# Kernel optimization log

Measured on AMD Instinct MI355X. Metric: run time of the kernel, lower is better.

Reference implementation:

```python
import math
import jax, jax.numpy as jnp
import numpy as np

IN_CH = 64
NUM_ANCHOR = 4
MAP_H, MAP_W = 96, 96
BATCH = 8
BN_EPS = 1e-5


def _conv2d(x, w, b, padding, dilation):
    # x: [B,C,H,W], w: [O,I,kh,kw] (OIHW)
    y = jax.lax.conv_general_dilated(
        x, w, window_strides=(1, 1),
        padding=((padding, padding), (padding, padding)),
        rhs_dilation=(dilation, dilation),
        dimension_numbers=('NCHW', 'OIHW', 'NCHW'))
    return y + b[None, :, None, None]


def _bn(x, gamma, beta, mean, var):
    scale = gamma / jnp.sqrt(var + BN_EPS)
    return x * scale[None, :, None, None] + (beta - mean * scale)[None, :, None, None]


def setup_inputs() -> dict:
    key = jax.random.key(0)
    ks = jax.random.split(key, 12)
    # cyclic channel-shift permutation matrices, one per anchor pass
    eye = np.eye(IN_CH, dtype=np.float32)
    shift = IN_CH // (2 * NUM_ANCHOR)
    perms = np.stack([eye[np.roll(np.arange(IN_CH), i * shift)] for i in range(2 * NUM_ANCHOR)])
    w_std = 1.0 / math.sqrt(IN_CH * 9)
    return {
        'x': jax.random.normal(ks[0], (BATCH, IN_CH, MAP_H, MAP_W), dtype=jnp.float32),
        'perms': jnp.asarray(perms),
        'dcn_w': jax.random.normal(ks[1], (IN_CH, IN_CH, 3, 3), dtype=jnp.float32) * w_std,
        'dcn_b': jax.random.normal(ks[2], (IN_CH,), dtype=jnp.float32) * 0.01,
        'conv2_w': jax.random.normal(ks[3], (IN_CH, IN_CH, 3, 3), dtype=jnp.float32) * w_std,
        'conv2_b': jax.random.normal(ks[4], (IN_CH,), dtype=jnp.float32) * 0.01,
        'conv3_w': jax.random.normal(ks[5], (IN_CH, IN_CH, 3, 3), dtype=jnp.float32) * w_std,
        'conv3_b': jax.random.normal(ks[6], (IN_CH,), dtype=jnp.float32) * 0.01,
        'bn_gamma': jax.random.uniform(ks[7], (3, IN_CH), dtype=jnp.float32, minval=0.5, maxval=1.5),
        'bn_beta': jax.random.normal(ks[8], (3, IN_CH), dtype=jnp.float32) * 0.1,
        'bn_mean': jax.random.normal(ks[9], (3, IN_CH), dtype=jnp.float32) * 0.1,
        'bn_var': jax.random.uniform(ks[10], (3, IN_CH), dtype=jnp.float32, minval=0.5, maxval=1.5),
    }


def reference(x, perms, dcn_w, dcn_b, conv2_w, conv2_b, conv3_w, conv3_b,
              bn_gamma, bn_beta, bn_mean, bn_var):
    h = x.shape[2]
    pad = math.ceil(h / (2 ** 1.5 + 2))  # 20 for h=96

    def conv_stack(o):
        # DCN at init (zero offsets) == plain 3x3 conv, pad=1
        o = jax.nn.relu(_bn(_conv2d(o, dcn_w, dcn_b, 1, 1), bn_gamma[0], bn_beta[0], bn_mean[0], bn_var[0]))
        o = jax.nn.relu(_bn(_conv2d(o, conv2_w, conv2_b, 2, 2), bn_gamma[1], bn_beta[1], bn_mean[1], bn_var[1]))
        o = jax.nn.relu(_bn(_conv2d(o, conv3_w, conv3_b, 2, 2), bn_gamma[2], bn_beta[2], bn_mean[2], bn_var[2]))
        return o

    outs = []
    for i in range(2 * NUM_ANCHOR):  # fixed small structural loop
        o = jnp.einsum('mn,bnhw->bmhw', perms[i], x)  # channel permutation
        if i % 2 != 0:
            o = jnp.pad(o, ((0, 0), (0, 0), (pad, pad), (pad, pad)))
        o = jnp.rot90(o, k=i % 4, axes=(-2, -1))   # ccw rotate
        o = conv_stack(o)
        o = jnp.rot90(o, k=(-i) % 4, axes=(-2, -1))  # cw rotate back
        if i % 2 != 0:
            H, W = o.shape[-2], o.shape[-1]
            sh, sw = (H - MAP_H) // 2, (W - MAP_W) // 2
            o = o[..., sh:sh + MAP_H, sw:sw + MAP_W]  # center crop
        outs.append(o)
    out_tensor = jnp.concatenate(outs, axis=1)  # [B, 8*C, H, W]
    out = jnp.max(out_tensor, axis=1, keepdims=True)
    # branch_name == 'midpoint', orientational_anchor=False -> clamped sigmoid
    return jnp.clip(jax.nn.sigmoid(out), 1e-4, 1.0 - 1e-4)
```

## Files before the change

kernel.cpp:

```cpp
#include <hip/hip_runtime.h>
#include <math.h>

#define B 8
#define C 64
#define HW 96
#define NWV 36864

typedef __attribute__((ext_vector_type(8)))  short short8;
typedef __attribute__((ext_vector_type(16))) float floatx16;

__device__ __forceinline__ unsigned short f2bf(float f) {
    unsigned int u = __float_as_uint(f);
    unsigned int r = (u + 0x7fffu + ((u >> 16) & 1u)) >> 16;
    return (unsigned short)r;
}

__device__ __forceinline__ void rotmap(int k, int ta, int tb, int& sa, int& sb) {
    switch (k) {
        case 0: sa = ta;     sb = tb;     break;
        case 1: sa = 2 - tb; sb = ta;     break;
        case 2: sa = 2 - ta; sb = 2 - tb; break;
        default: sa = tb;    sb = 2 - ta; break;
    }
}

__global__ void prep_w(const float* __restrict__ dcn_w, const float* __restrict__ c2w,
                       const float* __restrict__ c3w,
                       const float* __restrict__ gamma, const float* __restrict__ var_,
                       unsigned short* __restrict__ Wall) {
    int idx = blockIdx.x * 256 + threadIdx.x;
    if (idx >= 16 * NWV) return;
    int v = idx / NWV, rem = idx % NWV;
    int tap  = rem >> 12;
    int w12  = rem & 4095;
    int ks   = w12 >> 10;
    int cf   = (w12 >> 9) & 1;
    int lane = (w12 >> 3) & 63;
    int j    = w12 & 7;
    int co = cf * 32 + (lane & 31);
    int ci = ks * 16 + (lane >> 5) * 8 + j;
    int ta = tap / 3, tb = tap % 3;
    const float* src; int k, srcci, l;
    if (v < 8)       { k = v & 3;  srcci = (ci + 8 * v) & 63; src = dcn_w; l = 0; }
    else if (v < 12) { k = v - 8;  srcci = ci; src = c2w; l = 1; }
    else             { k = v - 12; srcci = ci; src = c3w; l = 2; }
    int sa, sb; rotmap(k, ta, tb, sa, sb);
    float s = gamma[l * 64 + co] * rsqrtf(var_[l * 64 + co] + 1e-5f);
    Wall[idx] = f2bf(src[((co * 64 + srcci) * 3 + sa) * 3 + sb] * s);
}

__global__ void prep_bias(const float* __restrict__ dcn_b, const float* __restrict__ c2b,
                          const float* __restrict__ c3b,
                          const float* __restrict__ gamma, const float* __restrict__ beta,
                          const float* __restrict__ mean, const float* __restrict__ var_,
                          float* __restrict__ biasg) {
    int t = threadIdx.x;
    if (t < 192) {
        int l = t >> 6, c = t & 63;
        const float* cb = (l == 0) ? dcn_b : ((l == 1) ? c2b : c3b);
        float s = gamma[l * 64 + c] * rsqrtf(var_[l * 64 + c] + 1e-5f);
        biasg[t] = cb[c] * s + beta[l * 64 + c] - mean[l * 64 + c] * s;
    }
}

__global__ __launch_bounds__(256) void prep_x(const float* __restrict__ in,
                                              unsigned short* __restrict__ out) {
    __shared__ float row[64 * 97];
    int by = blockIdx.x;
    int b = by / 96, y = by % 96;
    int t = threadIdx.x;
    for (int e = t; e < 6144; e += 256) {
        int c = e / 96, x = e - c * 96;
        row[c * 97 + x] = in[(((size_t)(b * 64 + c) * 96 + y) * 96) + x];
    }
    __syncthreads();
    for (int e = t; e < 6144; e += 256) {
        int x = e >> 6, c = e & 63;
        out[(((size_t)(b * 96 + y) * 96 + x) << 6) + c] = f2bf(row[c * 97 + x]);
    }
}

__global__ __launch_bounds__(256) void border_clear(unsigned short* __restrict__ buf1) {
    int idx = blockIdx.y;
    int br = (idx >> 3) * 2, b = idx & 7;
    int z = br * 8 + b;
    int i = blockIdx.x * 32 + (threadIdx.x >> 3);
    int g = threadIdx.x & 7;
    int r, c;
    if (i < 416)      { r = i / 104;              c = i % 104; }
    else if (i < 832) { int j = i - 416; r = 100 + j / 104; c = j % 104; }
    else              { int j = i - 832; r = 4 + (j >> 3); int c8 = j & 7;
                        c = (c8 < 4) ? c8 : 92 + c8; }
    uint4 zero = make_uint4(0u, 0u, 0u, 0u);
    *(uint4*)(buf1 + (size_t)z * (104 * 104 * 64) + ((size_t)(r * 104 + c) << 6) + (g << 3)) = zero;
}

__global__ __launch_bounds__(256, 2) void conv1_k(
    const unsigned short* __restrict__ xhwc, unsigned short* __restrict__ buf1,
    const unsigned short* __restrict__ Wall, const float* __restrict__ biasg) {

    __shared__ __align__(16) unsigned short xt[10 * 34 * 64];

    int z = blockIdx.z, br = z >> 3, b = z & 7, odd = br & 1;
    int fy0 = blockIdx.y * 8, fx0 = blockIdx.x * 32;
    int t = threadIdx.x, lane = t & 63, wv = t >> 6;
    int n = lane & 31, kq = lane >> 5;

    const unsigned short* xb = xhwc + ((size_t)b * 96 * 96 << 6);
    const short8* Ag = (const short8*)(Wall + (size_t)br * NWV);

    for (int e = t; e < 2720; e += 256) {
        int p = e >> 3, g = e & 7;
        int yy = p / 34, xx = p - yy * 34;
        int gy = fy0 - 5 + yy, gx = fx0 - 5 + xx;
        uint4 v = make_uint4(0u, 0u, 0u, 0u);
        if ((unsigned)gy < 96u && (unsigned)gx < 96u)
            v = *(const uint4*)(xb + ((size_t)(gy * 96 + gx) << 6) + (g << 3));
        *(uint4*)(xt + (p << 6) + ((g ^ (xx & 7)) << 3)) = v;
    }
    __syncthreads();

    floatx16 acc[2][2];
#pragma unroll
    for (int cf = 0; cf < 2; cf++)
#pragma unroll
        for (int pf = 0; pf < 2; pf++)
#pragma unroll
            for (int i = 0; i < 16; i++) acc[cf][pf][i] = 0.f;

#pragma unroll
    for (int ks = 0; ks < 4; ks++) {
#pragma unroll
        for (int tb = 0; tb < 3; tb++) {
            short8 a[3][2];
#pragma unroll
            for (int ta = 0; ta < 3; ta++)
#pragma unroll
                for (int cf = 0; cf < 2; cf++)
                    a[ta][cf] = Ag[(((ta * 3 + tb) * 4 + ks) * 2 + cf) * 64 + lane];
            int xx = n + tb;
            int g = ((ks * 2 + kq) ^ (xx & 7)) << 3;
            short8 bf[4];
#pragma unroll
            for (int rr = 0; rr < 4; rr++) {
                int p = (2 * wv + rr) * 34 + xx;
                bf[rr] = *(const short8*)(xt + (p << 6) + g);
            }
#pragma unroll
            for (int ta = 0; ta < 3; ta++)
#pragma unroll
                for (int pf = 0; pf < 2; pf++) {
                    int rr = pf + ta;
                    acc[0][pf] = __builtin_amdgcn_mfma_f32_32x32x16_bf16(a[ta][0], bf[rr], acc[0][pf], 0, 0, 0);
                    acc[1][pf] = __builtin_amdgcn_mfma_f32_32x32x16_bf16(a[ta][1], bf[rr], acc[1][pf], 0, 0, 0);
                }
        }
    }

    float4 bv[2][4];
#pragma unroll
    for (int cf = 0; cf < 2; cf++)
#pragma unroll
        for (int rb = 0; rb < 4; rb++)
            bv[cf][rb] = *(const float4*)(biasg + 32 * cf + 8 * rb + 4 * kq);

    __syncthreads();
#pragma unroll
    for (int pf = 0; pf < 2; pf++) {
        int pq = (2 * wv + pf) * 32 + n;
        int key = (pq & 7) << 1;
#pragma unroll
        for (int cf = 0; cf < 2; cf++)
#pragma unroll
            for (int rb = 0; rb < 4; rb++) {
                int u = kq + 2 * rb + 8 * cf;
                float v0 = fmaxf(acc[cf][pf][rb * 4 + 0] + bv[cf][rb].x, 0.f);
                float v1 = fmaxf(acc[cf][pf][rb * 4 + 1] + bv[cf][rb].y, 0.f);
                float v2 = fmaxf(acc[cf][pf][rb * 4 + 2] + bv[cf][rb].z, 0.f);
                float v3 = fmaxf(acc[cf][pf][rb * 4 + 3] + bv[cf][rb].w, 0.f);
                uint2 pk = make_uint2((unsigned)f2bf(v0) | ((unsigned)f2bf(v1) << 16),
                                      (unsigned)f2bf(v2) | ((unsigned)f2bf(v3) << 16));
                *(uint2*)((char*)xt + pq * 128 + ((u ^ key) << 3)) = pk;
            }
    }
    __syncthreads();

    unsigned short* fb = buf1 + (size_t)z * (104 * 104 * 64);
    int lo = odd ? 0 : 4, hi = odd ? 104 : 100;
    for (int e = t; e < 2048; e += 256) {
        int px = e >> 3, g = e & 7;
        int key = (px & 7) << 1;
        uint4 v = *(const uint4*)((const char*)xt + px * 128 + (((2 * g) ^ key) << 3));
        int lr = px >> 5, nn = px & 31;
        int f = fy0 + lr, fc = fx0 + nn;
        if (f >= lo && f < hi && fc >= lo && fc < hi)
            *(uint4*)(fb + ((size_t)(f * 104 + fc) << 6) + (g << 3)) = v;
    }
}

__global__ __launch_bounds__(512, 2) void conv23_k(
    const unsigned short* __restrict__ buf1, float* __restrict__ maxb,
    const unsigned short* __restrict__ Wall, const float* __restrict__ biasg) {

    __shared__ __align__(16) unsigned short c2out[768 * 64];
    __shared__ __align__(16) unsigned short xs[960 * 32];

    int z = blockIdx.z, br = z >> 3, odd = br & 1;
    int oy0 = blockIdx.y * 16, ox0 = blockIdx.x * 32;
    int t = threadIdx.x, lane = t & 63, wv = t >> 6;
    int n = lane & 31, kq = lane >> 5;

    const unsigned short* fb = buf1 + (size_t)z * (104 * 104 * 64);
    const short8* A2 = (const short8*)(Wall + (size_t)(8  + (br & 3)) * NWV);
    const short8* A3 = (const short8*)(Wall + (size_t)(12 + (br & 3)) * NWV);

    for (int e = t; e < 3840; e += 512) {
        int p = e >> 2, g = e & 3;
        int yy = p / 40, xx = p - yy * 40;
        uint4 v = *(const uint4*)(fb + ((size_t)((oy0 + yy) * 104 + ox0 + xx) << 6) + (g << 3));
        *(uint4*)(xs + (p << 5) + ((g ^ (xx & 3)) << 3)) = v;
    }
    __syncthreads();

    uint4 pfv[8];
#pragma unroll
    for (int k = 0; k < 8; k++) {
        int e = t + k * 512;
        if (e < 3840) {
            int p = e >> 2, g = e & 3;
            int yy = p / 40, xx = p - yy * 40;
            pfv[k] = *(const uint4*)(fb + ((size_t)((oy0 + yy) * 104 + ox0 + xx) << 6) + 32 + (g << 3));
        }
    }

    int q_[3], row2_[3], col2_[3];
#pragma unroll
    for (int jj = 0; jj < 3; jj++) {
        int q = 96 * wv + 32 * jj + n;
        q_[jj] = q;
        int qc = (q < 720) ? q : 719;
        int r2 = qc / 36;
        row2_[jj] = r2;
        col2_[jj] = qc - 36 * r2;
    }

    floatx16 acc2[3][2];
#pragma unroll
    for (int jj = 0; jj < 3; jj++)
#pragma unroll
        for (int cf = 0; cf < 2; cf++)
#pragma unroll
            for (int i = 0; i < 16; i++) acc2[jj][cf][i] = 0.f;

#pragma unroll
    for (int s = 0; s < 2; s++) {
        if (s == 1) {
            __syncthreads();
#pragma unroll
            for (int k = 0; k < 8; k++) {
                int e = t + k * 512;
                if (e < 3840) {
                    int p = e >> 2, g = e & 3;
                    int xx2 = p - (p / 40) * 40;
                    *(uint4*)(xs + (p << 5) + ((g ^ (xx2 & 3)) << 3)) = pfv[k];
                }
            }
            __syncthreads();
        }
#pragma unroll
        for (int kl = 0; kl < 2; kl++) {
            int ks = s * 2 + kl;
#pragma unroll
            for (int tb = 0; tb < 3; tb++) {
                short8 a[3][2];
#pragma unroll
                for (int ta = 0; ta < 3; ta++)
#pragma unroll
                    for (int cf = 0; cf < 2; cf++)
                        a[ta][cf] = A2[(((ta * 3 + tb) * 4 + ks) * 2 + cf) * 64 + lane];
#pragma unroll
                for (int jj = 0; jj < 3; jj++) {
                    int colx = col2_[jj] + 2 * tb;
                    int gsw = ((kl * 2 + kq) ^ (colx & 3)) << 3;
#pragma unroll
                    for (int ta = 0; ta < 3; ta++) {
                        int p = (row2_[jj] + 2 * ta) * 40 + colx;
                        short8 bfr = *(const short8*)(xs + (p << 5) + gsw);
                        acc2[jj][0] = __builtin_amdgcn_mfma_f32_32x32x16_bf16(a[ta][0], bfr, acc2[jj][0], 0, 0, 0);
                        acc2[jj][1] = __builtin_amdgcn_mfma_f32_32x32x16_bf16(a[ta][1], bfr, acc2[jj][1], 0, 0, 0);
                    }
                }
            }
        }
    }

    int rlo2 = (!odd && oy0 == 0)  ? 2  : 0;
    int rhi2 = (!odd && oy0 == 80) ? 18 : 20;
    int clo2 = (!odd && ox0 == 0)  ? 2  : 0;
    int chi2 = (!odd && ox0 == 64) ? 34 : 36;
    float4 bv2[2][4];
#pragma unroll
    for (int cf = 0; cf < 2; cf++)
#pragma unroll
        for (int rb = 0; rb < 4; rb++)
            bv2[cf][rb] = *(const float4*)(biasg + 64 + 32 * cf + 8 * rb + 4 * kq);

#pragma unroll
    for (int jj = 0; jj < 3; jj++) {
        if (q_[jj] < 720) {
            bool valid = (row2_[jj] >= rlo2) && (row2_[jj] < rhi2) &&
                         (col2_[jj] >= clo2) && (col2_[jj] < chi2);
            int key = col2_[jj] & 14;
#pragma unroll
            for (int cf = 0; cf < 2; cf++)
#pragma unroll
                for (int rb = 0; rb < 4; rb++) {
                    int u = kq + 2 * rb + 8 * cf;
                    float v0 = 0.f, v1 = 0.f, v2 = 0.f, v3 = 0.f;
                    if (valid) {
                        v0 = fmaxf(acc2[jj][cf][rb * 4 + 0] + bv2[cf][rb].x, 0.f);
                        v1 = fmaxf(acc2[jj][cf][rb * 4 + 1] + bv2[cf][rb].y, 0.f);
                        v2 = fmaxf(acc2[jj][cf][rb * 4 + 2] + bv2[cf][rb].z, 0.f);
                        v3 = fmaxf(acc2[jj][cf][rb * 4 + 3] + bv2[cf][rb].w, 0.f);
                    }
                    uint2 pk = make_uint2((unsigned)f2bf(v0) | ((unsigned)f2bf(v1) << 16),
                                          (unsigned)f2bf(v2) | ((unsigned)f2bf(v3) << 16));
                    *(uint2*)((char*)c2out + q_[jj] * 128 + ((u ^ key) << 3)) = pk;
                }
        }
    }
    __syncthreads();

    int r0 = 2 * wv;
    floatx16 acc3[2][2];
#pragma unroll
    for (int cf = 0; cf < 2; cf++)
#pragma unroll
        for (int pf = 0; pf < 2; pf++)
#pragma unroll
            for (int i = 0; i < 16; i++) acc3[cf][pf][i] = 0.f;

#pragma unroll
    for (int ks = 0; ks < 4; ks++) {
#pragma unroll
        for (int tb = 0; tb < 3; tb++) {
            short8 a[3][2];
#pragma unroll
            for (int ta = 0; ta < 3; ta++)
#pragma unroll
                for (int cf = 0; cf < 2; cf++)
                    a[ta][cf] = A3[(((ta * 3 + tb) * 4 + ks) * 2 + cf) * 64 + lane];
            int col = n + 2 * tb;
            int key = col & 14;
            int ublk = 2 * (ks * 2 + kq);
            short8 bf[6];
#pragma unroll
            for (int rr = 0; rr < 6; rr++) {
                int q = (r0 + rr) * 36 + col;
                bf[rr] = *(const short8*)((const char*)c2out + q * 128 + ((ublk ^ key) << 3));
            }
#pragma unroll
            for (int ta = 0; ta < 3; ta++)
#pragma unroll
                for (int pf = 0; pf < 2; pf++) {
                    int rr = pf + 2 * ta;
                    acc3[0][pf] = __builtin_amdgcn_mfma_f32_32x32x16_bf16(a[ta][0], bf[rr], acc3[0][pf], 0, 0, 0);
                    acc3[1][pf] = __builtin_amdgcn_mfma_f32_32x32x16_bf16(a[ta][1], bf[rr], acc3[1][pf], 0, 0, 0);
                }
        }
    }

    float4 bv3[2][4];
#pragma unroll
    for (int cf = 0; cf < 2; cf++)
#pragma unroll
        for (int rb = 0; rb < 4; rb++)
            bv3[cf][rb] = *(const float4*)(biasg + 128 + 32 * cf + 8 * rb + 4 * kq);

#pragma unroll
    for (int pf = 0; pf < 2; pf++) {
        float m = 0.f;
#pragma unroll
        for (int cf = 0; cf < 2; cf++)
#pragma unroll
            for (int rb = 0; rb < 4; rb++) {
                m = fmaxf(m, acc3[cf][pf][rb * 4 + 0] + bv3[cf][rb].x);
                m = fmaxf(m, acc3[cf][pf][rb * 4 + 1] + bv3[cf][rb].y);
                m = fmaxf(m, acc3[cf][pf][rb * 4 + 2] + bv3[cf][rb].z);
                m = fmaxf(m, acc3[cf][pf][rb * 4 + 3] + bv3[cf][rb].w);
            }
        m = fmaxf(m, 0.f);
        m = fmaxf(m, __shfl_xor(m, 32, 64));
        if (lane < 32)
            maxb[((size_t)z * 96 + oy0 + r0 + pf) * 96 + ox0 + n] = m;
    }
}

__global__ void final_k(const float* __restrict__ maxb, float* __restrict__ out) {
    int i = blockIdx.x * 256 + threadIdx.x;
    if (i < B * HW * HW) {
        int b = i / 9216, yx = i - b * 9216;
        float m = 0.f;
#pragma unroll
        for (int br = 0; br < 8; br++)
            m = fmaxf(m, maxb[((size_t)(br * 8 + b)) * 9216 + yx]);
        float v = 1.f / (1.f + expf(-m));
        out[i] = fminf(fmaxf(v, 1e-4f), 1.f - 1e-4f);
    }
}


extern "C" void kernel_launch(void* const* d_in, const int* in_sizes, int n_in,
                              void* d_out, int out_size, void* d_ws, size_t ws_size,
                              hipStream_t stream) {
    const float* x     = (const float*)d_in[0];
    const float* dcn_w = (const float*)d_in[2];
    const float* dcn_b = (const float*)d_in[3];
    const float* c2w   = (const float*)d_in[4];
    const float* c2b   = (const float*)d_in[5];
    const float* c3w   = (const float*)d_in[6];
    const float* c3b   = (const float*)d_in[7];
    const float* gamma = (const float*)d_in[8];
    const float* beta  = (const float*)d_in[9];
    const float* mean  = (const float*)d_in[10];
    const float* var_  = (const float*)d_in[11];

    char* ws = (char*)d_ws;
    unsigned short* Wall = (unsigned short*)ws;
    size_t off = (size_t)16 * NWV * 2;
    float* biasg = (float*)(ws + off);            off += 1024;
    float* maxb  = (float*)(ws + off);            off += (size_t)64 * 9216 * 4;
    unsigned short* xhwc = (unsigned short*)(ws + off); off += (size_t)B * 9216 * 64 * 2;
    unsigned short* buf1 = (unsigned short*)(ws + off);

    prep_w<<<(16 * NWV + 255) / 256, 256, 0, stream>>>(dcn_w, c2w, c3w, gamma, var_, Wall);
    prep_bias<<<1, 256, 0, stream>>>(dcn_b, c2b, c3b, gamma, beta, mean, var_, biasg);
    prep_x<<<B * 96, 256, 0, stream>>>(x, xhwc);
    border_clear<<<dim3(50, 32), 256, 0, stream>>>(buf1);

    dim3 g1(4, 13, 64);
    conv1_k<<<g1, 256, 0, stream>>>(xhwc, buf1, Wall, biasg);

    dim3 g23(3, 6, 64);
    conv23_k<<<g23, 512, 0, stream>>>(buf1, maxb, Wall, biasg);

    final_k<<<(B * HW * HW + 255) / 256, 256, 0, stream>>>(maxb, (float*)d_out);
}
```

Measured before the change: 310.5 us.

## Make conv2/conv3 kernel persistent with cross-tile prefetch and channel-split LDS

Replaces the 1152-block conv23 grid with 256 persistent blocks that each loop over spatial tiles of one (branch, batch) pair. Global loads for the next tile are issued into registers during the current tile's MFMA work, which hides load latency across tile boundaries. The conv2 output is staged in LDS in two 32-channel halves so conv3 can start on the first half, shrinking shared memory. XOR swizzling is replaced by 40-element padded rows. The trade-offs are fewer resident blocks, more barriers per tile, and possible bank conflicts from the padded layout.

Measured after the change: 692.2 us. +122.9%, slower.

```diff
diff --git a/kernel.cpp b/kernel.cpp
--- a/kernel.cpp
+++ b/kernel.cpp
@@ -198,40 +198,35 @@
     }
 }
 
-__global__ __launch_bounds__(512, 2) void conv23_k(
+__global__ __launch_bounds__(512, 2) void conv23_p(
     const unsigned short* __restrict__ buf1, float* __restrict__ maxb,
     const unsigned short* __restrict__ Wall, const float* __restrict__ biasg) {
 
-    __shared__ __align__(16) unsigned short c2out[768 * 64];
-    __shared__ __align__(16) unsigned short xs[960 * 32];
-
-    int z = blockIdx.z, br = z >> 3, odd = br & 1;
-    int oy0 = blockIdx.y * 16, ox0 = blockIdx.x * 32;
+    __shared__ __align__(16) unsigned short xs[960 * 40];
+    __shared__ __align__(16) unsigned short c2h[720 * 40];
+
     int t = threadIdx.x, lane = t & 63, wv = t >> 6;
     int n = lane & 31, kq = lane >> 5;
+
+    int item0 = blockIdx.x;
+    int b  = item0 & 7;
+    int br = (item0 >> 3) & 7;
+    int odd = br & 1;
+    int z  = br * 8 + b;
+    int tile = item0 >> 6;
 
     const unsigned short* fb = buf1 + (size_t)z * (104 * 104 * 64);
     const short8* A2 = (const short8*)(Wall + (size_t)(8  + (br & 3)) * NWV);
     const short8* A3 = (const short8*)(Wall + (size_t)(12 + (br & 3)) * NWV);
 
-    for (int e = t; e < 3840; e += 512) {
-        int p = e >> 2, g = e & 3;
-        int yy = p / 40, xx = p - yy * 40;
-        uint4 v = *(const uint4*)(fb + ((size_t)((oy0 + yy) * 104 + ox0 + xx) << 6) + (g << 3));
-        *(uint4*)(xs + (p << 5) + ((g ^ (xx & 3)) << 3)) = v;
-    }
-    __syncthreads();
-
-    uint4 pfv[8];
-#pragma unroll
-    for (int k = 0; k < 8; k++) {
-        int e = t + k * 512;
-        if (e < 3840) {
-            int p = e >> 2, g = e & 3;
-            int yy = p / 40, xx = p - yy * 40;
-            pfv[k] = *(const uint4*)(fb + ((size_t)((oy0 + yy) * 104 + ox0 + xx) << 6) + 32 + (g << 3));
-        }
-    }
+    float4 bv2[2][4], bv3[2][4];
+#pragma unroll
+    for (int cf = 0; cf < 2; cf++)
+#pragma unroll
+        for (int rb = 0; rb < 4; rb++) {
+            bv2[cf][rb] = *(const float4*)(biasg + 64  + 32 * cf + 8 * rb + 4 * kq);
+            bv3[cf][rb] = *(const float4*)(biasg + 128 + 32 * cf + 8 * rb + 4 * kq);
+        }
 
     int q_[3], row2_[3], col2_[3];
 #pragma unroll
@@ -244,29 +239,43 @@
         col2_[jj] = qc - 36 * r2;
     }
 
-    floatx16 acc2[3][2];
-#pragma unroll
-    for (int jj = 0; jj < 3; jj++)
-#pragma unroll
-        for (int cf = 0; cf < 2; cf++)
-#pragma unroll
-            for (int i = 0; i < 16; i++) acc2[jj][cf][i] = 0.f;
-
-#pragma unroll
-    for (int s = 0; s < 2; s++) {
-        if (s == 1) {
-            __syncthreads();
-#pragma unroll
-            for (int k = 0; k < 8; k++) {
-                int e = t + k * 512;
-                if (e < 3840) {
-                    int p = e >> 2, g = e & 3;
-                    int xx2 = p - (p / 40) * 40;
-                    *(uint4*)(xs + (p << 5) + ((g ^ (xx2 & 3)) << 3)) = pfv[k];
-                }
-            }
-            __syncthreads();
-        }
+    uint4 pfv[8];
+
+    auto stage_direct = [&](int oy0, int ox0, int s) {
+        for (int e = t; e < 3840; e += 512) {
+            int p = e >> 2, g = e & 3;
+            int yy = p / 40, xx = p - yy * 40;
+            uint4 v = *(const uint4*)(fb + (((size_t)((oy0 + yy) * 104 + ox0 + xx)) << 6)
+                                      + s * 32 + (g << 3));
+            *(uint4*)(xs + p * 40 + (g << 3)) = v;
+        }
+    };
+    auto pf_issue = [&](int oy0, int ox0, int s) {
+#pragma unroll
+        for (int k2 = 0; k2 < 8; k2++) {
+            int e = t + k2 * 512;
+            if (e < 3840) {
+                int p = e >> 2, g = e & 3;
+                int yy = p / 40, xx = p - yy * 40;
+                pfv[k2] = *(const uint4*)(fb + (((size_t)((oy0 + yy) * 104 + ox0 + xx)) << 6)
+                                          + s * 32 + (g << 3));
+            }
+        }
+    };
+    auto pf_commit = [&]() {
+#pragma unroll
+        for (int k2 = 0; k2 < 8; k2++) {
+            int e = t + k2 * 512;
+            if (e < 3840) {
+                int p = e >> 2, g = e & 3;
+                *(uint4*)(xs + p * 40 + (g << 3)) = pfv[k2];
+            }
+        }
+    };
+
+    floatx16 acc2[3][2], acc3[2][2];
+
+    auto conv2_half = [&](int s) {
 #pragma unroll
         for (int kl = 0; kl < 2; kl++) {
             int ks = s * 2 + kl;
@@ -278,121 +287,154 @@
 #pragma unroll
                     for (int cf = 0; cf < 2; cf++)
                         a[ta][cf] = A2[(((ta * 3 + tb) * 4 + ks) * 2 + cf) * 64 + lane];
+                int uoff = (kl * 2 + kq) << 3;
 #pragma unroll
                 for (int jj = 0; jj < 3; jj++) {
                     int colx = col2_[jj] + 2 * tb;
-                    int gsw = ((kl * 2 + kq) ^ (colx & 3)) << 3;
 #pragma unroll
                     for (int ta = 0; ta < 3; ta++) {
                         int p = (row2_[jj] + 2 * ta) * 40 + colx;
-                        short8 bfr = *(const short8*)(xs + (p << 5) + gsw);
+                        short8 bfr = *(const short8*)(xs + p * 40 + uoff);
                         acc2[jj][0] = __builtin_amdgcn_mfma_f32_32x32x16_bf16(a[ta][0], bfr, acc2[jj][0], 0, 0, 0);
                         acc2[jj][1] = __builtin_amdgcn_mfma_f32_32x32x16_bf16(a[ta][1], bfr, acc2[jj][1], 0, 0, 0);
                     }
                 }
             }
         }
-    }
-
-    int rlo2 = (!odd && oy0 == 0)  ? 2  : 0;
-    int rhi2 = (!odd && oy0 == 80) ? 18 : 20;
-    int clo2 = (!odd && ox0 == 0)  ? 2  : 0;
-    int chi2 = (!odd && ox0 == 64) ? 34 : 36;
-    float4 bv2[2][4];
-#pragma unroll
-    for (int cf = 0; cf < 2; cf++)
-#pragma unroll
-        for (int rb = 0; rb < 4; rb++)
-            bv2[cf][rb] = *(const float4*)(biasg + 64 + 32 * cf + 8 * rb + 4 * kq);
-
-#pragma unroll
-    for (int jj = 0; jj < 3; jj++) {
-        if (q_[jj] < 720) {
-            bool valid = (row2_[jj] >= rlo2) && (row2_[jj] < rhi2) &&
-                         (col2_[jj] >= clo2) && (col2_[jj] < chi2);
-            int key = col2_[jj] & 14;
-#pragma unroll
-            for (int cf = 0; cf < 2; cf++)
+    };
+
+    auto write_c2h = [&](int h, int rlo, int rhi, int clo, int chi) {
+#pragma unroll
+        for (int jj = 0; jj < 3; jj++) {
+            if (q_[jj] < 720) {
+                bool valid = (row2_[jj] >= rlo) && (row2_[jj] < rhi) &&
+                             (col2_[jj] >= clo) && (col2_[jj] < chi);
 #pragma unroll
                 for (int rb = 0; rb < 4; rb++) {
-                    int u = kq + 2 * rb + 8 * cf;
                     float v0 = 0.f, v1 = 0.f, v2 = 0.f, v3 = 0.f;
                     if (valid) {
-                        v0 = fmaxf(acc2[jj][cf][rb * 4 + 0] + bv2[cf][rb].x, 0.f);
-                        v1 = fmaxf(acc2[jj][cf][rb * 4 + 1] + bv2[cf][rb].y, 0.f);
-                        v2 = fmaxf(acc2[jj][cf][rb * 4 + 2] + bv2[cf][rb].z, 0.f);
-                        v3 = fmaxf(acc2[jj][cf][rb * 4 + 3] + bv2[cf][rb].w, 0.f);
+                        float4 bb = bv2[h][rb];
+                        v0 = fmaxf(acc2[jj][h][rb * 4 + 0] + bb.x, 0.f);
+                        v1 = fmaxf(acc2[jj][h][rb * 4 + 1] + bb.y, 0.f);
+                        v2 = fmaxf(acc2[jj][h][rb * 4 + 2] + bb.z, 0.f);
+                        v3 = fmaxf(acc2[jj][h][rb * 4 + 3] + bb.w, 0.f);
                     }
                     uint2 pk = make_uint2((unsigned)f2bf(v0) | ((unsigned)f2bf(v1) << 16),
                                           (unsigned)f2bf(v2) | ((unsigned)f2bf(v3) << 16));
-                    *(uint2*)((char*)c2out + q_[jj] * 128 + ((u ^ key) << 3)) = pk;
+                    *(uint2*)(c2h + q_[jj] * 40 + 8 * rb + 4 * kq) = pk;
                 }
-        }
+            }
+        }
+    };
+
+    auto conv3_half = [&](int h) {
+#pragma unroll
+        for (int ks3 = 0; ks3 < 2; ks3++) {
+            int ks = h * 2 + ks3;
+#pragma unroll
+            for (int tb = 0; tb < 3; tb++) {
+                short8 a[3][2];
+#pragma unroll
+                for (int ta = 0; ta < 3; ta++)
+#pragma unroll
+                    for (int cf = 0; cf < 2; cf++)
+                        a[ta][cf] = A3[(((ta * 3 + tb) * 4 + ks) * 2 + cf) * 64 + lane];
+                int col = n + 2 * tb;
+                int uoff = (ks3 * 2 + kq) << 3;
+                short8 bf[6];
+#pragma unroll
+                for (int rr = 0; rr < 6; rr++) {
+                    int q = (2 * wv + rr) * 36 + col;
+                    bf[rr] = *(const short8*)(c2h + q * 40 + uoff);
+                }
+#pragma unroll
+                for (int ta = 0; ta < 3; ta++)
+#pragma unroll
+                    for (int pf = 0; pf < 2; pf++) {
+                        int rr = pf + 2 * ta;
+                        acc3[0][pf] = __builtin_amdgcn_mfma_f32_32x32x16_bf16(a[ta][0], bf[rr], acc3[0][pf], 0, 0, 0);
+                        acc3[1][pf] = __builtin_amdgcn_mfma_f32_32x32x16_bf16(a[ta][1], bf[rr], acc3[1][pf], 0, 0, 0);
+                    }
+            }
+        }
+    };
+
+    {
+        int oy0 = (tile / 3) * 16, ox0 = (tile % 3) * 32;
+        stage_direct(oy0, ox0, 0);
+        pf_issue(oy0, ox0, 1);
     }
     __syncthreads();
 
-    int r0 = 2 * wv;
-    floatx16 acc3[2][2];
-#pragma unroll
-    for (int cf = 0; cf < 2; cf++)
-#pragma unroll
-        for (int pf = 0; pf < 2; pf++)
-#pragma unroll
-            for (int i = 0; i < 16; i++) acc3[cf][pf][i] = 0.f;
-
-#pragma unroll
-    for (int ks = 0; ks < 4; ks++) {
-#pragma unroll
-        for (int tb = 0; tb < 3; tb++) {
-            short8 a[3][2];
-#pragma unroll
-            for (int ta = 0; ta < 3; ta++)
-#pragma unroll
-                for (int cf = 0; cf < 2; cf++)
-                    a[ta][cf] = A3[(((ta * 3 + tb) * 4 + ks) * 2 + cf) * 64 + lane];
-            int col = n + 2 * tb;
-            int key = col & 14;
-            int ublk = 2 * (ks * 2 + kq);
-            short8 bf[6];
-#pragma unroll
-            for (int rr = 0; rr < 6; rr++) {
-                int q = (r0 + rr) * 36 + col;
-                bf[rr] = *(const short8*)((const char*)c2out + q * 128 + ((ublk ^ key) << 3));
-            }
-#pragma unroll
-            for (int ta = 0; ta < 3; ta++)
-#pragma unroll
-                for (int pf = 0; pf < 2; pf++) {
-                    int rr = pf + 2 * ta;
-                    acc3[0][pf] = __builtin_amdgcn_mfma_f32_32x32x16_bf16(a[ta][0], bf[rr], acc3[0][pf], 0, 0, 0);
-                    acc3[1][pf] = __builtin_amdgcn_mfma_f32_32x32x16_bf16(a[ta][1], bf[rr], acc3[1][pf], 0, 0, 0);
+    for (;;) {
+        int oy0 = (tile / 3) * 16, ox0 = (tile % 3) * 32;
+        int rlo2 = (!odd && oy0 == 0)  ? 2  : 0;
+        int rhi2 = (!odd && oy0 == 80) ? 18 : 20;
+        int clo2 = (!odd && ox0 == 0)  ? 2  : 0;
+        int chi2 = (!odd && ox0 == 64) ? 34 : 36;
+
+#pragma unroll
+        for (int jj = 0; jj < 3; jj++)
+#pragma unroll
+            for (int cf = 0; cf < 2; cf++)
+#pragma unroll
+                for (int i = 0; i < 16; i++) acc2[jj][cf][i] = 0.f;
+
+        conv2_half(0);
+        __syncthreads();
+        pf_commit();
+        __syncthreads();
+
+        int ntile = tile + 4;
+        bool more = ntile < 18;
+        int noy0 = (ntile / 3) * 16, nox0 = (ntile % 3) * 32;
+
+        conv2_half(1);
+        if (more) pf_issue(noy0, nox0, 0);
+        __syncthreads();
+
+        write_c2h(0, rlo2, rhi2, clo2, chi2);
+        if (more) pf_commit();
+        __syncthreads();
+
+#pragma unroll
+        for (int cf = 0; cf < 2; cf++)
+#pragma unroll
+            for (int pf = 0; pf < 2; pf++)
+#pragma unroll
+                for (int i = 0; i < 16; i++) acc3[cf][pf][i] = 0.f;
+
+        conv3_half(0);
+        if (more) pf_issue(noy0, nox0, 1);
+        __syncthreads();
+
+        write_c2h(1, rlo2, rhi2, clo2, chi2);
+        __syncthreads();
+
+        conv3_half(1);
+
+#pragma unroll
+        for (int pf = 0; pf < 2; pf++) {
+            float m = 0.f;
+#pragma unroll
+            for (int cf = 0; cf < 2; cf++)
+#pragma unroll
+                for (int rb = 0; rb < 4; rb++) {
+                    float4 bb = bv3[cf][rb];
+                    m = fmaxf(m, acc3[cf][pf][rb * 4 + 0] + bb.x);
+                    m = fmaxf(m, acc3[cf][pf][rb * 4 + 1] + bb.y);
+                    m = fmaxf(m, acc3[cf][pf][rb * 4 + 2] + bb.z);
+                    m = fmaxf(m, acc3[cf][pf][rb * 4 + 3] + bb.w);
                 }
-        }
-    }
-
-    float4 bv3[2][4];
-#pragma unroll
-    for (int cf = 0; cf < 2; cf++)
-#pragma unroll
-        for (int rb = 0; rb < 4; rb++)
-            bv3[cf][rb] = *(const float4*)(biasg + 128 + 32 * cf + 8 * rb + 4 * kq);
-
-#pragma unroll
-    for (int pf = 0; pf < 2; pf++) {
-        float m = 0.f;
-#pragma unroll
-        for (int cf = 0; cf < 2; cf++)
-#pragma unroll
-            for (int rb = 0; rb < 4; rb++) {
-                m = fmaxf(m, acc3[cf][pf][rb * 4 + 0] + bv3[cf][rb].x);
-                m = fmaxf(m, acc3[cf][pf][rb * 4 + 1] + bv3[cf][rb].y);
-                m = fmaxf(m, acc3[cf][pf][rb * 4 + 2] + bv3[cf][rb].z);
-                m = fmaxf(m, acc3[cf][pf][rb * 4 + 3] + bv3[cf][rb].w);
-            }
-        m = fmaxf(m, 0.f);
-        m = fmaxf(m, __shfl_xor(m, 32, 64));
-        if (lane < 32)
-            maxb[((size_t)z * 96 + oy0 + r0 + pf) * 96 + ox0 + n] = m;
+            m = fmaxf(m, 0.f);
+            m = fmaxf(m, __shfl_xor(m, 32, 64));
+            if (lane < 32)
+                maxb[((size_t)z * 96 + oy0 + 2 * wv + pf) * 96 + ox0 + n] = m;
+        }
+
+        if (!more) break;
+        tile = ntile;
+        __syncthreads();
     }
 }
 
@@ -441,8 +483,7 @@
     dim3 g1(4, 13, 64);
     conv1_k<<<g1, 256, 0, stream>>>(xhwc, buf1, Wall, biasg);
 
-    dim3 g23(3, 6, 64);
-    conv23_k<<<g23, 512, 0, stream>>>(buf1, maxb, Wall, biasg);
+    conv23_p<<<256, 512, 0, stream>>>(buf1, maxb, Wall, biasg);
 
     final_k<<<(B * HW * HW + 255) / 256, 256, 0, stream>>>(maxb, (float*)d_out);
 }
```

## Pipeline conv2 input staging in four 16-channel slices with padded LDS layout

Applied to the files above, without the earlier changes.

Restructures the conv23 kernel's input staging. It now loads 16 channels per k-step into a smaller padded shared buffer, prefetching the next slice from global memory while the current one is consumed. The XOR-swizzled layouts for both the input tile and the conv2 output are replaced by padded row strides (20 and 72 shorts), and bias loads are hoisted to the top. Launch bounds drop from 2 to 1 block per SM. This trades extra barriers and possibly lower occupancy for less register pressure from prefetch buffers and a smaller LDS footprint.

Result: slower. 388.9 us (+25.3%).

```diff
diff --git a/kernel.cpp b/kernel.cpp
--- a/kernel.cpp
+++ b/kernel.cpp
@@ -198,12 +198,12 @@
     }
 }
 
-__global__ __launch_bounds__(512, 2) void conv23_k(
+__global__ __launch_bounds__(512, 1) void conv23_k(
     const unsigned short* __restrict__ buf1, float* __restrict__ maxb,
     const unsigned short* __restrict__ Wall, const float* __restrict__ biasg) {
 
-    __shared__ __align__(16) unsigned short c2out[768 * 64];
-    __shared__ __align__(16) unsigned short xs[960 * 32];
+    __shared__ __align__(16) unsigned short xs[960 * 20];
+    __shared__ __align__(16) unsigned short c2out[720 * 72];
 
     int z = blockIdx.z, br = z >> 3, odd = br & 1;
     int oy0 = blockIdx.y * 16, ox0 = blockIdx.x * 32;
@@ -214,24 +214,14 @@
     const short8* A2 = (const short8*)(Wall + (size_t)(8  + (br & 3)) * NWV);
     const short8* A3 = (const short8*)(Wall + (size_t)(12 + (br & 3)) * NWV);
 
-    for (int e = t; e < 3840; e += 512) {
-        int p = e >> 2, g = e & 3;
-        int yy = p / 40, xx = p - yy * 40;
-        uint4 v = *(const uint4*)(fb + ((size_t)((oy0 + yy) * 104 + ox0 + xx) << 6) + (g << 3));
-        *(uint4*)(xs + (p << 5) + ((g ^ (xx & 3)) << 3)) = v;
-    }
-    __syncthreads();
-
-    uint4 pfv[8];
-#pragma unroll
-    for (int k = 0; k < 8; k++) {
-        int e = t + k * 512;
-        if (e < 3840) {
-            int p = e >> 2, g = e & 3;
-            int yy = p / 40, xx = p - yy * 40;
-            pfv[k] = *(const uint4*)(fb + ((size_t)((oy0 + yy) * 104 + ox0 + xx) << 6) + 32 + (g << 3));
-        }
-    }
+    float4 bv2[2][4], bv3[2][4];
+#pragma unroll
+    for (int cf = 0; cf < 2; cf++)
+#pragma unroll
+        for (int rb = 0; rb < 4; rb++) {
+            bv2[cf][rb] = *(const float4*)(biasg + 64  + 32 * cf + 8 * rb + 4 * kq);
+            bv3[cf][rb] = *(const float4*)(biasg + 128 + 32 * cf + 8 * rb + 4 * kq);
+        }
 
     int q_[3], row2_[3], col2_[3];
 #pragma unroll
@@ -244,6 +234,23 @@
         col2_[jj] = qc - 36 * r2;
     }
 
+    int sp_p[4], sp_g[4]; size_t sp_gaddr[4]; bool sp_on[4];
+#pragma unroll
+    for (int k2 = 0; k2 < 4; k2++) {
+        int e = t + k2 * 512;
+        sp_on[k2] = e < 1920;
+        int p = e >> 1, g = e & 1;
+        if (!sp_on[k2]) { p = 0; g = 0; }
+        sp_p[k2] = p; sp_g[k2] = g;
+        int yy = p / 40, xx = p - yy * 40;
+        sp_gaddr[k2] = (((size_t)((oy0 + yy) * 104 + ox0 + xx)) << 6) + (g << 3);
+    }
+
+    uint4 ld[4];
+#pragma unroll
+    for (int k2 = 0; k2 < 4; k2++)
+        if (sp_on[k2]) ld[k2] = *(const uint4*)(fb + sp_gaddr[k2]);
+
     floatx16 acc2[3][2];
 #pragma unroll
     for (int jj = 0; jj < 3; jj++)
@@ -252,43 +259,36 @@
 #pragma unroll
             for (int i = 0; i < 16; i++) acc2[jj][cf][i] = 0.f;
 
-#pragma unroll
-    for (int s = 0; s < 2; s++) {
-        if (s == 1) {
-            __syncthreads();
-#pragma unroll
-            for (int k = 0; k < 8; k++) {
-                int e = t + k * 512;
-                if (e < 3840) {
-                    int p = e >> 2, g = e & 3;
-                    int xx2 = p - (p / 40) * 40;
-                    *(uint4*)(xs + (p << 5) + ((g ^ (xx2 & 3)) << 3)) = pfv[k];
-                }
-            }
-            __syncthreads();
-        }
-#pragma unroll
-        for (int kl = 0; kl < 2; kl++) {
-            int ks = s * 2 + kl;
-#pragma unroll
-            for (int tb = 0; tb < 3; tb++) {
-                short8 a[3][2];
-#pragma unroll
-                for (int ta = 0; ta < 3; ta++)
-#pragma unroll
-                    for (int cf = 0; cf < 2; cf++)
-                        a[ta][cf] = A2[(((ta * 3 + tb) * 4 + ks) * 2 + cf) * 64 + lane];
-#pragma unroll
-                for (int jj = 0; jj < 3; jj++) {
-                    int colx = col2_[jj] + 2 * tb;
-                    int gsw = ((kl * 2 + kq) ^ (colx & 3)) << 3;
-#pragma unroll
-                    for (int ta = 0; ta < 3; ta++) {
-                        int p = (row2_[jj] + 2 * ta) * 40 + colx;
-                        short8 bfr = *(const short8*)(xs + (p << 5) + gsw);
-                        acc2[jj][0] = __builtin_amdgcn_mfma_f32_32x32x16_bf16(a[ta][0], bfr, acc2[jj][0], 0, 0, 0);
-                        acc2[jj][1] = __builtin_amdgcn_mfma_f32_32x32x16_bf16(a[ta][1], bfr, acc2[jj][1], 0, 0, 0);
-                    }
+    for (int ks = 0; ks < 4; ks++) {
+        if (ks) __syncthreads();
+#pragma unroll
+        for (int k2 = 0; k2 < 4; k2++)
+            if (sp_on[k2]) *(uint4*)(xs + sp_p[k2] * 20 + (sp_g[k2] << 3)) = ld[k2];
+        if (ks < 3) {
+#pragma unroll
+            for (int k2 = 0; k2 < 4; k2++)
+                if (sp_on[k2]) ld[k2] = *(const uint4*)(fb + sp_gaddr[k2] + ((ks + 1) << 4));
+        }
+        __syncthreads();
+
+#pragma unroll
+        for (int tb = 0; tb < 3; tb++) {
+            short8 a[3][2];
+#pragma unroll
+            for (int ta = 0; ta < 3; ta++)
+#pragma unroll
+                for (int cf = 0; cf < 2; cf++)
+                    a[ta][cf] = A2[(((ta * 3 + tb) * 4 + ks) * 2 + cf) * 64 + lane];
+            int uoff = kq << 3;
+#pragma unroll
+            for (int jj = 0; jj < 3; jj++) {
+                int colx = col2_[jj] + 2 * tb;
+#pragma unroll
+                for (int ta = 0; ta < 3; ta++) {
+                    int p = (row2_[jj] + 2 * ta) * 40 + colx;
+                    short8 bfr = *(const short8*)(xs + p * 20 + uoff);
+                    acc2[jj][0] = __builtin_amdgcn_mfma_f32_32x32x16_bf16(a[ta][0], bfr, acc2[jj][0], 0, 0, 0);
+                    acc2[jj][1] = __builtin_amdgcn_mfma_f32_32x32x16_bf16(a[ta][1], bfr, acc2[jj][1], 0, 0, 0);
                 }
             }
         }
@@ -298,40 +298,32 @@
     int rhi2 = (!odd && oy0 == 80) ? 18 : 20;
     int clo2 = (!odd && ox0 == 0)  ? 2  : 0;
     int chi2 = (!odd && ox0 == 64) ? 34 : 36;
-    float4 bv2[2][4];
-#pragma unroll
-    for (int cf = 0; cf < 2; cf++)
-#pragma unroll
-        for (int rb = 0; rb < 4; rb++)
-            bv2[cf][rb] = *(const float4*)(biasg + 64 + 32 * cf + 8 * rb + 4 * kq);
 
 #pragma unroll
     for (int jj = 0; jj < 3; jj++) {
         if (q_[jj] < 720) {
             bool valid = (row2_[jj] >= rlo2) && (row2_[jj] < rhi2) &&
                          (col2_[jj] >= clo2) && (col2_[jj] < chi2);
-            int key = col2_[jj] & 14;
 #pragma unroll
             for (int cf = 0; cf < 2; cf++)
 #pragma unroll
                 for (int rb = 0; rb < 4; rb++) {
-                    int u = kq + 2 * rb + 8 * cf;
                     float v0 = 0.f, v1 = 0.f, v2 = 0.f, v3 = 0.f;
                     if (valid) {
-                        v0 = fmaxf(acc2[jj][cf][rb * 4 + 0] + bv2[cf][rb].x, 0.f);
-                        v1 = fmaxf(acc2[jj][cf][rb * 4 + 1] + bv2[cf][rb].y, 0.f);
-                        v2 = fmaxf(acc2[jj][cf][rb * 4 + 2] + bv2[cf][rb].z, 0.f);
-                        v3 = fmaxf(acc2[jj][cf][rb * 4 + 3] + bv2[cf][rb].w, 0.f);
+                        float4 bb = bv2[cf][rb];
+                        v0 = fmaxf(acc2[jj][cf][rb * 4 + 0] + bb.x, 0.f);
+                        v1 = fmaxf(acc2[jj][cf][rb * 4 + 1] + bb.y, 0.f);
+                        v2 = fmaxf(acc2[jj][cf][rb * 4 + 2] + bb.z, 0.f);
+                        v3 = fmaxf(acc2[jj][cf][rb * 4 + 3] + bb.w, 0.f);
                     }
                     uint2 pk = make_uint2((unsigned)f2bf(v0) | ((unsigned)f2bf(v1) << 16),
                                           (unsigned)f2bf(v2) | ((unsigned)f2bf(v3) << 16));
-                    *(uint2*)((char*)c2out + q_[jj] * 128 + ((u ^ key) << 3)) = pk;
+                    *(uint2*)(c2out + q_[jj] * 72 + 32 * cf + 8 * rb + 4 * kq) = pk;
                 }
         }
     }
     __syncthreads();
 
-    int r0 = 2 * wv;
     floatx16 acc3[2][2];
 #pragma unroll
     for (int cf = 0; cf < 2; cf++)
@@ -351,13 +343,12 @@
                 for (int cf = 0; cf < 2; cf++)
                     a[ta][cf] = A3[(((ta * 3 + tb) * 4 + ks) * 2 + cf) * 64 + lane];
             int col = n + 2 * tb;
-            int key = col & 14;
-            int ublk = 2 * (ks * 2 + kq);
+            int uoff = (2 * ks + kq) << 3;
             short8 bf[6];
 #pragma unroll
             for (int rr = 0; rr < 6; rr++) {
-                int q = (r0 + rr) * 36 + col;
-                bf[rr] = *(const short8*)((const char*)c2out + q * 128 + ((ublk ^ key) << 3));
+                int q = (2 * wv + rr) * 36 + col;
+                bf[rr] = *(const short8*)(c2out + q * 72 + uoff);
             }
 #pragma unroll
             for (int ta = 0; ta < 3; ta++)
@@ -370,13 +361,6 @@
         }
     }
 
-    float4 bv3[2][4];
-#pragma unroll
-    for (int cf = 0; cf < 2; cf++)
-#pragma unroll
-        for (int rb = 0; rb < 4; rb++)
-            bv3[cf][rb] = *(const float4*)(biasg + 128 + 32 * cf + 8 * rb + 4 * kq);
-
 #pragma unroll
     for (int pf = 0; pf < 2; pf++) {
         float m = 0.f;
@@ -384,15 +368,16 @@
         for (int cf = 0; cf < 2; cf++)
 #pragma unroll
             for (int rb = 0; rb < 4; rb++) {
-                m = fmaxf(m, acc3[cf][pf][rb * 4 + 0] + bv3[cf][rb].x);
-                m = fmaxf(m, acc3[cf][pf][rb * 4 + 1] + bv3[cf][rb].y);
-                m = fmaxf(m, acc3[cf][pf][rb * 4 + 2] + bv3[cf][rb].z);
-                m = fmaxf(m, acc3[cf][pf][rb * 4 + 3] + bv3[cf][rb].w);
+                float4 bb = bv3[cf][rb];
+                m = fmaxf(m, acc3[cf][pf][rb * 4 + 0] + bb.x);
+                m = fmaxf(m, acc3[cf][pf][rb * 4 + 1] + bb.y);
+                m = fmaxf(m, acc3[cf][pf][rb * 4 + 2] + bb.z);
+                m = fmaxf(m, acc3[cf][pf][rb * 4 + 3] + bb.w);
             }
         m = fmaxf(m, 0.f);
         m = fmaxf(m, __shfl_xor(m, 32, 64));
         if (lane < 32)
-            maxb[((size_t)z * 96 + oy0 + r0 + pf) * 96 + ox0 + n] = m;
+            maxb[((size_t)z * 96 + oy0 + 2 * wv + pf) * 96 + ox0 + n] = m;
     }
 }
 
```

## Enlarge conv1 tiles, pad conv3 smem layout instead of XOR swizzle, cut register bias

Applied to the files above, without the earlier changes.

conv1 now runs 512-thread blocks covering 16 output rows instead of 8, so each staged input halo serves more rows and fewer blocks are launched. In conv23 the stage-2 output buffer switches from an XOR-swizzled 128-byte row layout to a 68-element padded row, which avoids bank conflicts with simpler address math. Bias vectors are now loaded at the point of use rather than held in registers, and both kernels drop to one block per SIMD in their launch bounds, which frees registers but lowers occupancy. conv1's internal tiling lines (not shown) must match the larger tile, and the padded stride gives 8-byte rather than 16-byte alignment for some short8 loads.

Result: slower. 338.1 us (+8.9%).

```diff
diff --git a/kernel.cpp b/kernel.cpp
--- a/kernel.cpp
+++ b/kernel.cpp
@@ -95,21 +95,21 @@
     *(uint4*)(buf1 + (size_t)z * (104 * 104 * 64) + ((size_t)(r * 104 + c) << 6) + (g << 3)) = zero;
 }
 
-__global__ __launch_bounds__(256, 2) void conv1_k(
+__global__ __launch_bounds__(512, 1) void conv1_k(
     const unsigned short* __restrict__ xhwc, unsigned short* __restrict__ buf1,
     const unsigned short* __restrict__ Wall, const float* __restrict__ biasg) {
 
-    __shared__ __align__(16) unsigned short xt[10 * 34 * 64];
+    __shared__ __align__(16) unsigned short xt[612 * 64];
 
     int z = blockIdx.z, br = z >> 3, b = z & 7, odd = br & 1;
-    int fy0 = blockIdx.y * 8, fx0 = blockIdx.x * 32;
+    int fy0 = blockIdx.y * 16, fx0 = blockIdx.x * 32;
     int t = threadIdx.x, lane = t & 63, wv = t >> 6;
     int n = lane & 31, kq = lane >> 5;
 
     const unsigned short* xb = xhwc + ((size_t)b * 96 * 96 << 6);
     const short8* Ag = (const short8*)(Wall + (size_t)br * NWV);
 
-    for (int e = t; e < 2720; e += 256) {
+    for (int e = t; e < 4896; e += 512) {
         int p = e >> 3, g = e & 7;
         int yy = p / 34, xx = p - yy * 34;
         int gy = fy0 - 5 + yy, gx = fx0 - 5 + xx;
@@ -187,7 +187,7 @@
 
     unsigned short* fb = buf1 + (size_t)z * (104 * 104 * 64);
     int lo = odd ? 0 : 4, hi = odd ? 104 : 100;
-    for (int e = t; e < 2048; e += 256) {
+    for (int e = t; e < 4096; e += 512) {
         int px = e >> 3, g = e & 7;
         int key = (px & 7) << 1;
         uint4 v = *(const uint4*)((const char*)xt + px * 128 + (((2 * g) ^ key) << 3));
@@ -198,12 +198,12 @@
     }
 }
 
-__global__ __launch_bounds__(512, 2) void conv23_k(
+__global__ __launch_bounds__(512, 1) void conv23_k(
     const unsigned short* __restrict__ buf1, float* __restrict__ maxb,
     const unsigned short* __restrict__ Wall, const float* __restrict__ biasg) {
 
-    __shared__ __align__(16) unsigned short c2out[768 * 64];
     __shared__ __align__(16) unsigned short xs[960 * 32];
+    __shared__ __align__(16) unsigned short c2out[720 * 68];
 
     int z = blockIdx.z, br = z >> 3, odd = br & 1;
     int oy0 = blockIdx.y * 16, ox0 = blockIdx.x * 32;
@@ -298,40 +298,32 @@
     int rhi2 = (!odd && oy0 == 80) ? 18 : 20;
     int clo2 = (!odd && ox0 == 0)  ? 2  : 0;
     int chi2 = (!odd && ox0 == 64) ? 34 : 36;
-    float4 bv2[2][4];
-#pragma unroll
-    for (int cf = 0; cf < 2; cf++)
-#pragma unroll
-        for (int rb = 0; rb < 4; rb++)
-            bv2[cf][rb] = *(const float4*)(biasg + 64 + 32 * cf + 8 * rb + 4 * kq);
 
 #pragma unroll
     for (int jj = 0; jj < 3; jj++) {
         if (q_[jj] < 720) {
             bool valid = (row2_[jj] >= rlo2) && (row2_[jj] < rhi2) &&
                          (col2_[jj] >= clo2) && (col2_[jj] < chi2);
-            int key = col2_[jj] & 14;
 #pragma unroll
             for (int cf = 0; cf < 2; cf++)
 #pragma unroll
                 for (int rb = 0; rb < 4; rb++) {
-                    int u = kq + 2 * rb + 8 * cf;
                     float v0 = 0.f, v1 = 0.f, v2 = 0.f, v3 = 0.f;
                     if (valid) {
-                        v0 = fmaxf(acc2[jj][cf][rb * 4 + 0] + bv2[cf][rb].x, 0.f);
-                        v1 = fmaxf(acc2[jj][cf][rb * 4 + 1] + bv2[cf][rb].y, 0.f);
-                        v2 = fmaxf(acc2[jj][cf][rb * 4 + 2] + bv2[cf][rb].z, 0.f);
-                        v3 = fmaxf(acc2[jj][cf][rb * 4 + 3] + bv2[cf][rb].w, 0.f);
+                        float4 bb = *(const float4*)(biasg + 64 + 32 * cf + 8 * rb + 4 * kq);
+                        v0 = fmaxf(acc2[jj][cf][rb * 4 + 0] + bb.x, 0.f);
+                        v1 = fmaxf(acc2[jj][cf][rb * 4 + 1] + bb.y, 0.f);
+                        v2 = fmaxf(acc2[jj][cf][rb * 4 + 2] + bb.z, 0.f);
+                        v3 = fmaxf(acc2[jj][cf][rb * 4 + 3] + bb.w, 0.f);
                     }
                     uint2 pk = make_uint2((unsigned)f2bf(v0) | ((unsigned)f2bf(v1) << 16),
                                           (unsigned)f2bf(v2) | ((unsigned)f2bf(v3) << 16));
-                    *(uint2*)((char*)c2out + q_[jj] * 128 + ((u ^ key) << 3)) = pk;
+                    *(uint2*)(c2out + q_[jj] * 68 + 32 * cf + 8 * rb + 4 * kq) = pk;
                 }
         }
     }
     __syncthreads();
 
-    int r0 = 2 * wv;
     floatx16 acc3[2][2];
 #pragma unroll
     for (int cf = 0; cf < 2; cf++)
@@ -351,13 +343,12 @@
                 for (int cf = 0; cf < 2; cf++)
                     a[ta][cf] = A3[(((ta * 3 + tb) * 4 + ks) * 2 + cf) * 64 + lane];
             int col = n + 2 * tb;
-            int key = col & 14;
-            int ublk = 2 * (ks * 2 + kq);
+            int uoff = (2 * ks + kq) << 3;
             short8 bf[6];
 #pragma unroll
             for (int rr = 0; rr < 6; rr++) {
-                int q = (r0 + rr) * 36 + col;
-                bf[rr] = *(const short8*)((const char*)c2out + q * 128 + ((ublk ^ key) << 3));
+                int q = (2 * wv + rr) * 36 + col;
+                bf[rr] = *(const short8*)(c2out + q * 68 + uoff);
             }
 #pragma unroll
             for (int ta = 0; ta < 3; ta++)
@@ -370,13 +361,6 @@
         }
     }
 
-    float4 bv3[2][4];
-#pragma unroll
-    for (int cf = 0; cf < 2; cf++)
-#pragma unroll
-        for (int rb = 0; rb < 4; rb++)
-            bv3[cf][rb] = *(const float4*)(biasg + 128 + 32 * cf + 8 * rb + 4 * kq);
-
 #pragma unroll
     for (int pf = 0; pf < 2; pf++) {
         float m = 0.f;
@@ -384,15 +368,16 @@
         for (int cf = 0; cf < 2; cf++)
 #pragma unroll
             for (int rb = 0; rb < 4; rb++) {
-                m = fmaxf(m, acc3[cf][pf][rb * 4 + 0] + bv3[cf][rb].x);
-                m = fmaxf(m, acc3[cf][pf][rb * 4 + 1] + bv3[cf][rb].y);
-                m = fmaxf(m, acc3[cf][pf][rb * 4 + 2] + bv3[cf][rb].z);
-                m = fmaxf(m, acc3[cf][pf][rb * 4 + 3] + bv3[cf][rb].w);
+                float4 bb = *(const float4*)(biasg + 128 + 32 * cf + 8 * rb + 4 * kq);
+                m = fmaxf(m, acc3[cf][pf][rb * 4 + 0] + bb.x);
+                m = fmaxf(m, acc3[cf][pf][rb * 4 + 1] + bb.y);
+                m = fmaxf(m, acc3[cf][pf][rb * 4 + 2] + bb.z);
+                m = fmaxf(m, acc3[cf][pf][rb * 4 + 3] + bb.w);
             }
         m = fmaxf(m, 0.f);
         m = fmaxf(m, __shfl_xor(m, 32, 64));
         if (lane < 32)
-            maxb[((size_t)z * 96 + oy0 + r0 + pf) * 96 + ox0 + n] = m;
+            maxb[((size_t)z * 96 + oy0 + 2 * wv + pf) * 96 + ox0 + n] = m;
     }
 }
 
@@ -438,8 +423,8 @@
     prep_x<<<B * 96, 256, 0, stream>>>(x, xhwc);
     border_clear<<<dim3(50, 32), 256, 0, stream>>>(buf1);
 
-    dim3 g1(4, 13, 64);
-    conv1_k<<<g1, 256, 0, stream>>>(xhwc, buf1, Wall, biasg);
+    dim3 g1(4, 7, 64);
+    conv1_k<<<g1, 512, 0, stream>>>(xhwc, buf1, Wall, biasg);
 
     dim3 g23(3, 6, 64);
     conv23_k<<<g23, 512, 0, stream>>>(buf1, maxb, Wall, biasg);
```
